# Kernel optimization log

Measured on AMD Instinct MI355X. Metric: run time of the kernel, lower is better.

## Reference

```python
import jax, jax.numpy as jnp
import numpy as np
from jax import lax

B, CIN, L, COUT, K = 64, 64, 4096, 128, 7
STRIDE, PAD = 1, 3
POOL, POOL_STRIDE = 2, 2
BN_EPS = 1e-5


def setup_inputs() -> dict:
    key = jax.random.key(0)
    ks = jax.random.split(key, 7)
    I = jax.random.normal(ks[0], (B, CIN, L), jnp.float32)
    bn_gamma = 1.0 + 0.1 * jax.random.normal(ks[1], (CIN,), jnp.float32)
    bn_beta = 0.1 * jax.random.normal(ks[2], (CIN,), jnp.float32)
    bn_mean = 0.1 * jax.random.normal(ks[3], (CIN,), jnp.float32)
    bn_var = jax.random.uniform(ks[4], (CIN,), jnp.float32, 0.5, 1.5)
    conv_w = 0.05 * jax.random.normal(ks[5], (COUT, CIN, K), jnp.float32)
    # XNOR-Net style per-output-channel scale alpha = mean(|W|) over (Cin, K)
    alpha = jnp.mean(jnp.abs(conv_w), axis=(1, 2))  # [COUT]
    prelu_w = jnp.full((1,), 0.25, jnp.float32)  # nn.PReLU() default: 1 shared param
    return dict(I=I, bn_gamma=bn_gamma, bn_beta=bn_beta, bn_mean=bn_mean,
                bn_var=bn_var, conv_w=conv_w, alpha=alpha, prelu_w=prelu_w)


def reference(I, bn_gamma, bn_beta, bn_mean, bn_var, conv_w, alpha, prelu_w):
    # BatchNorm1d (eval mode: running stats), per-channel over dim 1
    scale = (bn_gamma / jnp.sqrt(bn_var + BN_EPS))[None, :, None]
    x = (I - bn_mean[None, :, None]) * scale + bn_beta[None, :, None]
    # Binarize (sign; sign(0)=0 matches torch.sign)
    x = jnp.sign(x)
    # Conv1d, no bias, zero padding=3, stride=1  -> [B, COUT, L]
    y = lax.conv_general_dilated(x, conv_w, window_strides=(STRIDE,),
                                 padding=[(PAD, PAD)],
                                 dimension_numbers=('NCH', 'OIH', 'NCH'))
    # alpha scale (per output channel)
    y = y * alpha[None, :, None]
    # PReLU with single shared parameter
    y = jnp.where(y > 0, y, prelu_w[0] * y)
    # MaxPool1d(kernel=2, stride=2)
    y = lax.reduce_window(y, -jnp.inf, lax.max,
                          (1, 1, POOL), (1, 1, POOL_STRIDE), 'VALID')
    return y
```

## Files before the change

### kernel.cpp

```cpp
#include <hip/hip_runtime.h>
#include <hip/hip_bf16.h>
#include <stdint.h>

#define BATCH 64
#define CIN   64
#define LEN   4096
#define COUT  128
#define KW    7
#define LPOOL 2048
#define RROWS 72

typedef __bf16 v8bf __attribute__((ext_vector_type(8)));
typedef unsigned short v8us __attribute__((ext_vector_type(8)));
typedef float  v4f  __attribute__((ext_vector_type(4)));

__global__ __launch_bounds__(256)
void wconv_kernel(const float* __restrict__ W, ushort* __restrict__ Wt) {
    int i = blockIdx.x * 256 + threadIdx.x;
    if (i >= COUT * CIN * KW) return;
    int co  = i / (CIN * KW);
    int rem = i - co * (CIN * KW);
    int ci  = rem / KW;
    int k   = rem - ci * KW;
    uint u = __float_as_uint(W[i]);
    uint r = (u + 0x7FFFu + ((u >> 16) & 1u)) >> 16;
    Wt[(k * COUT + co) * CIN + ci] = (ushort)r;
}

__global__ __launch_bounds__(256, 4)
void conv_kernel(const float* __restrict__ I,
                 const float* __restrict__ bn_g, const float* __restrict__ bn_b,
                 const float* __restrict__ bn_m, const float* __restrict__ bn_v,
                 const ushort* __restrict__ Wt,
                 const float* __restrict__ alpha, const float* __restrict__ prelu,
                 float* __restrict__ out) {
    __shared__ __align__(16) ushort stg[RROWS * 72];
    __shared__ float4 bnc[CIN];

    int tid = threadIdx.x;
    int b = blockIdx.y, l0 = blockIdx.x * 64;

    if (tid < CIN) {
        float s = __fdiv_rn(bn_g[tid], __fsqrt_rn(__fadd_rn(bn_v[tid], 1e-5f)));
        bnc[tid] = make_float4(s, bn_m[tid], bn_b[tid], 0.f);
    }
    __syncthreads();

    int g = tid >> 5;
    int rbase = tid & 31;
    float sc[8], mu[8], be[8];
    #pragma unroll
    for (int j = 0; j < 8; ++j) {
        float4 c = bnc[8 * g + j];
        sc[j] = c.x; mu[j] = c.y; be[j] = c.z;
    }

    const float* Ib = I + (size_t)b * CIN * LEN + (size_t)g * 8 * LEN;
    float v[3][8];
    bool inb[3];
    #pragma unroll
    for (int it = 0; it < 3; ++it) {
        int r = rbase + 32 * it;
        int p = l0 - 4 + r;
        inb[it] = (r < RROWS) && (p >= 0) && (p < LEN);
        #pragma unroll
        for (int j = 0; j < 8; ++j)
            v[it][j] = inb[it] ? Ib[j * LEN + p] : 0.f;
    }
    #pragma unroll
    for (int it = 0; it < 3; ++it) {
        int r = rbase + 32 * it;
        if (r < RROWS) {
            v8us u;
            #pragma unroll
            for (int j = 0; j < 8; ++j) {
                float x = __fadd_rn(__fmul_rn(__fsub_rn(v[it][j], mu[j]), sc[j]), be[j]);
                ushort s = x > 0.f ? (ushort)0x3F80 : (x < 0.f ? (ushort)0xBF80 : (ushort)0);
                if (!inb[it]) s = 0;
                u[j] = s;
            }
            *(v8us*)(stg + r * 72 + g * 8) = u;
        }
    }
    __syncthreads();

    int lane = tid & 63, wave = tid >> 6;
    int quad = lane >> 4, lr = lane & 15;
    int cout0 = wave * 32;

    v4f acc[4][2];
    #pragma unroll
    for (int mt = 0; mt < 4; ++mt) { acc[mt][0] = (v4f)0.f; acc[mt][1] = (v4f)0.f; }

    #pragma unroll
    for (int k = 0; k < KW; ++k) {
        #pragma unroll
        for (int h = 0; h < 2; ++h) {
            int cibase = h * 32 + quad * 8;
            const ushort* wrow = Wt + ((size_t)(k * COUT) + cout0 + lr) * CIN + cibase;
            v8bf b0 = *(const v8bf*)(wrow);
            v8bf b1 = *(const v8bf*)(wrow + 16 * CIN);
            #pragma unroll
            for (int mt = 0; mt < 4; ++mt) {
                v8bf a = *(const v8bf*)(stg + (mt * 16 + lr + k + 1) * 72 + cibase);
                acc[mt][0] = __builtin_amdgcn_mfma_f32_16x16x32_bf16(a, b0, acc[mt][0], 0, 0, 0);
                acc[mt][1] = __builtin_amdgcn_mfma_f32_16x16x32_bf16(a, b1, acc[mt][1], 0, 0, 0);
            }
        }
    }

    float pw = prelu[0];
    float* ob = out + ((size_t)b * COUT) * LPOOL + blockIdx.x * 32;
    #pragma unroll
    for (int nt = 0; nt < 2; ++nt) {
        int co = cout0 + nt * 16 + lr;
        float al = alpha[co];
        float* oc = ob + (size_t)co * LPOOL + quad * 2;
        #pragma unroll
        for (int mt = 0; mt < 4; ++mt) {
            float v0 = acc[mt][nt][0] * al; v0 = v0 > 0.f ? v0 : pw * v0;
            float v1 = acc[mt][nt][1] * al; v1 = v1 > 0.f ? v1 : pw * v1;
            float v2 = acc[mt][nt][2] * al; v2 = v2 > 0.f ? v2 : pw * v2;
            float v3 = acc[mt][nt][3] * al; v3 = v3 > 0.f ? v3 : pw * v3;
            *(float2*)(oc + mt * 8) = make_float2(fmaxf(v0, v1), fmaxf(v2, v3));
        }
    }
}

extern "C" void kernel_launch(void* const* d_in, const int* in_sizes, int n_in,
                              void* d_out, int out_size, void* d_ws, size_t ws_size,
                              hipStream_t stream) {
    const float* I      = (const float*)d_in[0];
    const float* bn_g   = (const float*)d_in[1];
    const float* bn_b   = (const float*)d_in[2];
    const float* bn_m   = (const float*)d_in[3];
    const float* bn_v   = (const float*)d_in[4];
    const float* conv_w = (const float*)d_in[5];
    const float* alpha  = (const float*)d_in[6];
    const float* prelu  = (const float*)d_in[7];
    float* out = (float*)d_out;

    ushort* Wt = (ushort*)d_ws;

    wconv_kernel<<<(COUT * CIN * KW + 255) / 256, 256, 0, stream>>>(conv_w, Wt);
    dim3 grid(LEN / 64, BATCH);
    conv_kernel<<<grid, 256, 0, stream>>>(I, bn_g, bn_b, bn_m, bn_v, Wt, alpha, prelu, out);
}
```

Before: 187.0 us.

## Process four length tiles per block with double-buffered LDS and prefetched input

Each block now covers four consecutive 64-position tiles instead of one. The next tile's input is loaded into registers while the current tile's MFMAs run, and it is binarized into a second LDS buffer. Weights for the next kernel tap are prefetched inside the k loop. The aim is to hide global load latency and amortize the BN setup. In exchange the grid shrinks fourfold (1024 blocks), register pressure rises, and each tile adds extra syncthreads.

```diff
diff --git a/kernel.cpp b/kernel.cpp
--- a/kernel.cpp
+++ b/kernel.cpp
@@ -9,6 +9,7 @@
 #define KW    7
 #define LPOOL 2048
 #define RROWS 72
+#define NT    4
 
 typedef __bf16 v8bf __attribute__((ext_vector_type(8)));
 typedef unsigned short v8us __attribute__((ext_vector_type(8)));
@@ -34,11 +35,12 @@
                  const ushort* __restrict__ Wt,
                  const float* __restrict__ alpha, const float* __restrict__ prelu,
                  float* __restrict__ out) {
-    __shared__ __align__(16) ushort stg[RROWS * 72];
+    __shared__ __align__(16) ushort stg[2][RROWS * 72];
     __shared__ float4 bnc[CIN];
 
     int tid = threadIdx.x;
-    int b = blockIdx.y, l0 = blockIdx.x * 64;
+    int b = blockIdx.y, bx = blockIdx.x;
+    int l0base = bx * (64 * NT);
 
     if (tid < CIN) {
         float s = __fdiv_rn(bn_g[tid], __fsqrt_rn(__fadd_rn(bn_v[tid], 1e-5f)));
@@ -48,82 +50,118 @@
 
     int g = tid >> 5;
     int rbase = tid & 31;
-    float sc[8], mu[8], be[8];
-    #pragma unroll
-    for (int j = 0; j < 8; ++j) {
-        float4 c = bnc[8 * g + j];
-        sc[j] = c.x; mu[j] = c.y; be[j] = c.z;
-    }
+    const float* Ib = I + (size_t)b * CIN * LEN + (size_t)g * 8 * LEN;
 
-    const float* Ib = I + (size_t)b * CIN * LEN + (size_t)g * 8 * LEN;
     float v[3][8];
     bool inb[3];
-    #pragma unroll
-    for (int it = 0; it < 3; ++it) {
-        int r = rbase + 32 * it;
-        int p = l0 - 4 + r;
-        inb[it] = (r < RROWS) && (p >= 0) && (p < LEN);
+
+    auto stage_regs = [&](int t) {
+        int l0 = l0base + t * 64;
         #pragma unroll
-        for (int j = 0; j < 8; ++j)
-            v[it][j] = inb[it] ? Ib[j * LEN + p] : 0.f;
-    }
-    #pragma unroll
-    for (int it = 0; it < 3; ++it) {
-        int r = rbase + 32 * it;
-        if (r < RROWS) {
-            v8us u;
+        for (int it = 0; it < 3; ++it) {
+            int r = rbase + 32 * it;
+            int p = l0 - 4 + r;
+            inb[it] = (r < RROWS) && (p >= 0) && (p < LEN);
             #pragma unroll
-            for (int j = 0; j < 8; ++j) {
-                float x = __fadd_rn(__fmul_rn(__fsub_rn(v[it][j], mu[j]), sc[j]), be[j]);
-                ushort s = x > 0.f ? (ushort)0x3F80 : (x < 0.f ? (ushort)0xBF80 : (ushort)0);
-                if (!inb[it]) s = 0;
-                u[j] = s;
+            for (int j = 0; j < 8; ++j)
+                v[it][j] = inb[it] ? Ib[j * LEN + p] : 0.f;
+        }
+    };
+    auto binwrite = [&](int buf) {
+        #pragma unroll
+        for (int it = 0; it < 3; ++it) {
+            int r = rbase + 32 * it;
+            if (r < RROWS) {
+                v8us u;
+                #pragma unroll
+                for (int j = 0; j < 8; ++j) {
+                    float4 c = bnc[8 * g + j];
+                    float x = __fadd_rn(__fmul_rn(__fsub_rn(v[it][j], c.y), c.x), c.z);
+                    ushort s = x > 0.f ? (ushort)0x3F80 : (x < 0.f ? (ushort)0xBF80 : (ushort)0);
+                    if (!inb[it]) s = 0;
+                    u[j] = s;
+                }
+                *(v8us*)(&stg[buf][r * 72 + g * 8]) = u;
             }
-            *(v8us*)(stg + r * 72 + g * 8) = u;
         }
-    }
-    __syncthreads();
+    };
 
     int lane = tid & 63, wave = tid >> 6;
     int quad = lane >> 4, lr = lane & 15;
     int cout0 = wave * 32;
+    const ushort* wbase = Wt + ((size_t)cout0 + lr) * CIN + quad * 8;
+
+    float pw  = prelu[0];
+    float al0 = alpha[cout0 + lr];
+    float al1 = alpha[cout0 + 16 + lr];
+    float* obase = out + ((size_t)b * COUT) * LPOOL + bx * (32 * NT);
 
     v4f acc[4][2];
-    #pragma unroll
-    for (int mt = 0; mt < 4; ++mt) { acc[mt][0] = (v4f)0.f; acc[mt][1] = (v4f)0.f; }
 
-    #pragma unroll
-    for (int k = 0; k < KW; ++k) {
+    stage_regs(0);
+    binwrite(0);
+    __syncthreads();
+
+    for (int t = 0; t < NT; ++t) {
+        if (t + 1 < NT) stage_regs(t + 1);
+
         #pragma unroll
-        for (int h = 0; h < 2; ++h) {
-            int cibase = h * 32 + quad * 8;
-            const ushort* wrow = Wt + ((size_t)(k * COUT) + cout0 + lr) * CIN + cibase;
-            v8bf b0 = *(const v8bf*)(wrow);
-            v8bf b1 = *(const v8bf*)(wrow + 16 * CIN);
+        for (int mt = 0; mt < 4; ++mt) { acc[mt][0] = (v4f)0.f; acc[mt][1] = (v4f)0.f; }
+
+        v8bf wcur[2][2], wnxt[2][2];
+        #pragma unroll
+        for (int h = 0; h < 2; ++h)
+            #pragma unroll
+            for (int n2 = 0; n2 < 2; ++n2)
+                wcur[h][n2] = *(const v8bf*)(wbase + h * 32 + n2 * 16 * CIN);
+
+        int buf = t & 1;
+        #pragma unroll
+        for (int k = 0; k < KW; ++k) {
+            if (k + 1 < KW) {
+                const ushort* wk = wbase + (size_t)(k + 1) * COUT * CIN;
+                #pragma unroll
+                for (int h = 0; h < 2; ++h)
+                    #pragma unroll
+                    for (int n2 = 0; n2 < 2; ++n2)
+                        wnxt[h][n2] = *(const v8bf*)(wk + h * 32 + n2 * 16 * CIN);
+            }
+            #pragma unroll
+            for (int h = 0; h < 2; ++h) {
+                int cibase = h * 32 + quad * 8;
+                #pragma unroll
+                for (int mt = 0; mt < 4; ++mt) {
+                    v8bf a = *(const v8bf*)(&stg[buf][(mt * 16 + lr + k + 1) * 72 + cibase]);
+                    acc[mt][0] = __builtin_amdgcn_mfma_f32_16x16x32_bf16(a, wcur[h][0], acc[mt][0], 0, 0, 0);
+                    acc[mt][1] = __builtin_amdgcn_mfma_f32_16x16x32_bf16(a, wcur[h][1], acc[mt][1], 0, 0, 0);
+                }
+            }
+            #pragma unroll
+            for (int h = 0; h < 2; ++h)
+                #pragma unroll
+                for (int n2 = 0; n2 < 2; ++n2)
+                    wcur[h][n2] = wnxt[h][n2];
+        }
+        __syncthreads();
+
+        if (t + 1 < NT) binwrite((t + 1) & 1);
+
+        float* ob = obase + t * 32;
+        #pragma unroll
+        for (int n2 = 0; n2 < 2; ++n2) {
+            float al = n2 ? al1 : al0;
+            int co = cout0 + n2 * 16 + lr;
+            float* oc = ob + (size_t)co * LPOOL + quad * 2;
             #pragma unroll
             for (int mt = 0; mt < 4; ++mt) {
-                v8bf a = *(const v8bf*)(stg + (mt * 16 + lr + k + 1) * 72 + cibase);
-                acc[mt][0] = __builtin_amdgcn_mfma_f32_16x16x32_bf16(a, b0, acc[mt][0], 0, 0, 0);
-                acc[mt][1] = __builtin_amdgcn_mfma_f32_16x16x32_bf16(a, b1, acc[mt][1], 0, 0, 0);
+                float v0 = acc[mt][n2][0] * al; v0 = v0 > 0.f ? v0 : pw * v0;
+                float v1 = acc[mt][n2][1] * al; v1 = v1 > 0.f ? v1 : pw * v1;
+                float v2 = acc[mt][n2][2] * al; v2 = v2 > 0.f ? v2 : pw * v2;
+                float v3 = acc[mt][n2][3] * al; v3 = v3 > 0.f ? v3 : pw * v3;
+                *(float2*)(oc + mt * 8) = make_float2(fmaxf(v0, v1), fmaxf(v2, v3));
             }
         }
-    }
-
-    float pw = prelu[0];
-    float* ob = out + ((size_t)b * COUT) * LPOOL + blockIdx.x * 32;
-    #pragma unroll
-    for (int nt = 0; nt < 2; ++nt) {
-        int co = cout0 + nt * 16 + lr;
-        float al = alpha[co];
-        float* oc = ob + (size_t)co * LPOOL + quad * 2;
-        #pragma unroll
-        for (int mt = 0; mt < 4; ++mt) {
-            float v0 = acc[mt][nt][0] * al; v0 = v0 > 0.f ? v0 : pw * v0;
-            float v1 = acc[mt][nt][1] * al; v1 = v1 > 0.f ? v1 : pw * v1;
-            float v2 = acc[mt][nt][2] * al; v2 = v2 > 0.f ? v2 : pw * v2;
-            float v3 = acc[mt][nt][3] * al; v3 = v3 > 0.f ? v3 : pw * v3;
-            *(float2*)(oc + mt * 8) = make_float2(fmaxf(v0, v1), fmaxf(v2, v3));
-        }
+        __syncthreads();
     }
 }
 
@@ -143,6 +181,6 @@
     ushort* Wt = (ushort*)d_ws;
 
     wconv_kernel<<<(COUT * CIN * KW + 255) / 256, 256, 0, stream>>>(conv_w, Wt);
-    dim3 grid(LEN / 64, BATCH);
+    dim3 grid(LEN / (64 * NT), BATCH);
     conv_kernel<<<grid, 256, 0, stream>>>(I, bn_g, bn_b, bn_m, bn_v, Wt, alpha, prelu, out);
 }
```

Result: slower. 273.2 us (+46.1%).
